# Optimization experiments

Measured on AMD Instinct MI355X. Metric: run time of the kernel, lower is better.

Reference implementation:

```python
import jax, jax.numpy as jnp
import numpy as np

B, T, M, P, N2 = 16, 8192, 128, 128, 128  # N2 = N//2 complex modes

def setup_inputs() -> dict:
    key = jax.random.key(0)
    k1, k2, k3, k4, k5 = jax.random.split(key, 5)
    u = jax.random.normal(k1, (B, T, M), dtype=jnp.float32)
    # log-parametrized Lambda (S5 'log' convention): Lambda = -exp(row0) + 1j*row1
    log_re = jnp.log(jax.random.uniform(k2, (N2,), minval=0.1, maxval=1.0))
    im = jnp.pi * jnp.arange(N2, dtype=jnp.float32)  # HiPPO-like imaginary spread
    Lambda_param = jnp.stack([log_re, im], axis=0).astype(jnp.float32)
    B_param = jax.random.normal(k3, (2, N2, M), dtype=jnp.float32) / np.sqrt(M)
    C_param = jax.random.normal(k4, (2, P, N2), dtype=jnp.float32) / np.sqrt(N2)
    delta = jnp.array([0.01], dtype=jnp.float32)  # default_\u0394
    return {"u": u, "Lambda_param": Lambda_param, "B_param": B_param,
            "C_param": C_param, "delta": delta}

def reference(u, Lambda_param, B_param, C_param, delta):
    # Reconstruct complex continuous-time matrices
    Lam = (-jnp.exp(Lambda_param[0]) + 1j * Lambda_param[1]).astype(jnp.complex64)   # (N2,)
    Bc = (B_param[0] + 1j * B_param[1]).astype(jnp.complex64)                        # (N2, M)
    Cc = (C_param[0] + 1j * C_param[1]).astype(jnp.complex64)                        # (P, N2)
    d = delta[0]
    # ZOH discretization: Lambda_d = exp(Lam*d), Bd = ((Lambda_d - 1)/Lam) * B
    Ld = jnp.exp(Lam * d)                                                            # (N2,)
    Bd = ((Ld - 1.0) / Lam)[:, None] * Bc                                            # (N2, M)
    # Input projection: Bu[b,t,n] = sum_m u[b,t,m] * Bd[n,m]
    Bu = jnp.einsum('btm,nm->btn', u.astype(jnp.complex64), Bd)                      # (B,T,N2)
    # Parallel scan of x_{k+1} = Ld * x_k + Bu_k, x_0 = 0 -> x holds x_1..x_T
    A = jnp.broadcast_to(Ld, Bu.shape)
    def comb(e1, e2):
        a1, b1 = e1
        a2, b2 = e2
        return (a1 * a2, a2 * b1 + b2)
    _, x = jax.lax.associative_scan(comb, (A, Bu), axis=1)                           # (B,T,N2)
    # return_next_y=True: y_k = 2*Re(C x_{k+1})
    y = 2.0 * jnp.real(jnp.einsum('btn,pn->btp', x, Cc))                             # (B,T,P)
    return y
```

## Files before the change

kernel.cpp:

```cpp
#include <hip/hip_runtime.h>
#include <hip/hip_bf16.h>

#define LCH 128
#define NCH 64
#define NCHUNKS 1024

typedef __attribute__((ext_vector_type(8))) short short8v;
typedef __attribute__((ext_vector_type(4))) short short4v;
typedef __attribute__((ext_vector_type(4))) float f32x4;

#define W2_LDINV 0
#define W2_LDP   16384
#define W2_E     32768
#define W2_CIN   163840
#define WS_WPACK_BYTE  2359296
#define WS_CCPACK_BYTE (2359296 + 65536)
#define WS_BUS_BYTE    (2359296 + 131072)
#define WS_NEED ((size_t)WS_BUS_BYTE + (size_t)NCHUNKS * 65536)

#define BUS_BYTE(s, np) ((((s) >> 3) * 4096) + ((np) * 16) + (((s) & 7) * 2))

__device__ inline unsigned short f2bf(float f) {
    union { __hip_bfloat16 h; unsigned short u; } v;
    v.h = __float2bfloat16(f);
    return v.u;
}
__device__ inline short4v pack4(float a, float b, float c, float d) {
    union { __hip_bfloat162 h2[2]; short4v s4; } pk;
    pk.h2[0] = __float22bfloat162_rn(make_float2(a, b));
    pk.h2[1] = __float22bfloat162_rn(make_float2(c, d));
    return pk.s4;
}

__global__ void k0_pows(const float* __restrict__ lp, const float* __restrict__ delta,
                        float2* __restrict__ ws2) {
    const int r = blockIdx.x;
    const int tid = threadIdx.x;
    const int n = tid & 127;
    const double d = (double)delta[0];
    const double lre = -exp((double)lp[n]);
    const double lim = (double)lp[128 + n];
    const double kk = (double)(r + 1) * d;
    if (tid < 128) {
        const double mag = exp(-lre * kk);
        ws2[W2_LDINV + r * 128 + n] = make_float2((float)(mag * cos(lim * kk)),
                                                  (float)(-mag * sin(lim * kk)));
    } else {
        const double mag = exp(lre * kk);
        ws2[W2_LDP + r * 128 + n] = make_float2((float)(mag * cos(lim * kk)),
                                                (float)(mag * sin(lim * kk)));
    }
}

__global__ void k0_wpack(const float* __restrict__ lp, const float* __restrict__ bp,
                         const float* __restrict__ delta, unsigned short* __restrict__ wpack) {
    const int gid = blockIdx.x * 512 + threadIdx.x;
    const int j = gid & 7;
    const int lane = (gid >> 3) & 63;
    const int ks = (gid >> 9) & 3;
    const int ntile = gid >> 11;
    const int np = ntile * 16 + (lane & 15);
    const int m = ks * 32 + ((lane >> 4) & 3) * 8 + j;
    const int n = np & 127;
    const double d = (double)delta[0];
    const double lre = -exp((double)lp[n]);
    const double lim = (double)lp[128 + n];
    const double er = exp(lre * d);
    const double ldr = er * cos(lim * d), ldi = er * sin(lim * d);
    const double nr = ldr - 1.0, ni = ldi;
    const double den = lre * lre + lim * lim;
    const double cr = (nr * lre + ni * lim) / den;
    const double ci = (ni * lre - nr * lim) / den;
    const double br = (double)bp[n * 128 + m];
    const double bi = (double)bp[16384 + n * 128 + m];
    const double v = (np < 128) ? (cr * br - ci * bi) : (cr * bi + ci * br);
    wpack[gid] = f2bf((float)v);
}

__global__ void k0_cpack(const float* __restrict__ cp, unsigned short* __restrict__ ccpack) {
    const int gid = blockIdx.x * 512 + threadIdx.x;
    const int j = gid & 7;
    const int lane = (gid >> 3) & 63;
    const int ks = (gid >> 9) & 7;
    const int ptile = gid >> 12;
    const int p = ptile * 16 + (lane & 15);
    const int k = ks * 32 + ((lane >> 4) & 3) * 8 + j;
    const int n = k >> 1;
    const float v = ((k & 1) == 0) ? 2.0f * cp[p * 128 + n] : -2.0f * cp[16384 + p * 128 + n];
    ccpack[gid] = f2bf(v);
}

__device__ inline void stage_u(const float* __restrict__ uchunk, unsigned short* lds_u) {
    const float4* uf = (const float4*)uchunk;
    const int tid = threadIdx.x;
#pragma unroll
    for (int it = 0; it < 8; ++it) {
        const int f4 = it * 512 + tid;
        const float4 v = uf[f4];
        const int t = f4 >> 5;
        const int m = (f4 & 31) * 4;
        const int byte = (t * 256 + m * 2) ^ ((t & 7) << 4);
        *(short4v*)((char*)lds_u + byte) = pack4(v.x, v.y, v.z, v.w);
    }
}

__global__ __launch_bounds__(512, 6) void k3a_bus(const float* __restrict__ u,
                                                  float2* __restrict__ ws2,
                                                  const unsigned short* __restrict__ wpack,
                                                  char* __restrict__ busg) {
    __shared__ unsigned short lds_u[16384];
    const int tid = threadIdx.x;
    const int lane = tid & 63;
    const int w = tid >> 6;
    const int tl = lane & 15;
    const int gq = (lane >> 4) & 3;
    const int g = blockIdx.x;
    const int b = g >> 6;
    const int c = g & 63;
    const int n = w * 16 + tl;
    const short8v* wp = (const short8v*)wpack;
    char* busc = busg + (size_t)g * 65536;

    stage_u(u + (size_t)(b * 8192 + c * 128) * 128, lds_u);
    __syncthreads();

    float er = 0.f, ei = 0.f;
#pragma unroll
    for (int h = 0; h < 2; ++h) {
        f32x4 acc[4][2];
#pragma unroll
        for (int i = 0; i < 4; ++i) { acc[i][0] = (f32x4)0.f; acc[i][1] = (f32x4)0.f; }
        __builtin_amdgcn_s_setprio(1);
#pragma unroll
        for (int ks = 0; ks < 4; ++ks) {
            const short8v b0 = wp[(w * 4 + ks) * 64 + lane];
            const short8v b1 = wp[((8 + w) * 4 + ks) * 64 + lane];
#pragma unroll
            for (int tt2 = 0; tt2 < 4; ++tt2) {
                const int t = (h * 4 + tt2) * 16 + tl;
                const int byte = (t * 256 + (ks * 32 + gq * 8) * 2) ^ ((t & 7) << 4);
                const short8v a = *(const short8v*)((const char*)lds_u + byte);
                acc[tt2][0] = __builtin_amdgcn_mfma_f32_16x16x32_bf16(a, b0, acc[tt2][0], 0, 0, 0);
                acc[tt2][1] = __builtin_amdgcn_mfma_f32_16x16x32_bf16(a, b1, acc[tt2][1], 0, 0, 0);
            }
        }
        __builtin_amdgcn_s_setprio(0);
        __builtin_amdgcn_sched_barrier(0);
#pragma unroll
        for (int tt2 = 0; tt2 < 4; ++tt2) {
            float vr[4], vi[4];
#pragma unroll
            for (int reg = 0; reg < 4; ++reg) {
                const int r = (h * 4 + tt2) * 16 + gq * 4 + reg;
                const float2 li = ws2[W2_LDINV + r * 128 + n];
                const float br = acc[tt2][0][reg], bi = acc[tt2][1][reg];
                vr[reg] = li.x * br - li.y * bi;
                vi[reg] = li.x * bi + li.y * br;
                er += vr[reg];
                ei += vi[reg];
            }
            const int s0 = (h * 4 + tt2) * 16 + gq * 4;
            const int rowr = w * 16 + tl;
            const int rowi = 128 + rowr;
            *(short4v*)(busc + BUS_BYTE(s0, rowr)) = pack4(vr[0], vr[1], vr[2], vr[3]);
            *(short4v*)(busc + BUS_BYTE(s0, rowi)) = pack4(vi[0], vi[1], vi[2], vi[3]);
        }
        __builtin_amdgcn_sched_barrier(0);
    }
    er += __shfl_xor(er, 16); ei += __shfl_xor(ei, 16);
    er += __shfl_xor(er, 32); ei += __shfl_xor(ei, 32);
    const float2 ld = ws2[W2_LDP + 127 * 128 + n];
    if (lane < 16) {
        ws2[W2_E + g * 128 + n] = make_float2(ld.x * er - ld.y * ei,
                                              ld.x * ei + ld.y * er);
    }
}

__global__ void k2_carry(float2* __restrict__ ws2) {
    const int idx = blockIdx.x * 256 + threadIdx.x;
    const int b = idx >> 7;
    const int n = idx & 127;
    const float2 l = ws2[W2_LDP + 127 * 128 + n];
    float cr = 0.f, ci = 0.f;
    for (int c = 0; c < NCH; ++c) {
        const int o = (b * NCH + c) * 128 + n;
        ws2[W2_CIN + o] = make_float2(cr, ci);
        const float2 e = ws2[W2_E + o];
        const float nr = fmaf(l.x, cr, fmaf(-l.y, ci, e.x));
        const float ni = fmaf(l.x, ci, fmaf(l.y, cr, e.y));
        cr = nr; ci = ni;
    }
}

__global__ __launch_bounds__(512, 4) void k3b_out(const float2* __restrict__ ws2,
                                                  const char* __restrict__ busg,
                                                  const unsigned short* __restrict__ ccpack,
                                                  float* __restrict__ y) {
    __shared__ unsigned short lds[32768];
    const int tid = threadIdx.x;
    const int lane = tid & 63;
    const int w = tid >> 6;
    const int tl = lane & 15;
    const int gq = (lane >> 4) & 3;
    const int g = blockIdx.x;
    const int b = g >> 6;
    const int c = g & 63;
    const int n = w * 16 + tl;
    const short8v* cc8 = (const short8v*)ccpack;
    const char* busc = busg + (size_t)g * 65536;

    short8v ONES, D0, D1;
#pragma unroll
    for (int j = 0; j < 8; ++j) {
        const int sl = gq * 8 + j;
        ONES[j] = (short)0x3F80;
        D0[j] = (sl <= tl) ? (short)0x3F80 : (short)0;
        D1[j] = (sl <= tl + 16) ? (short)0x3F80 : (short)0;
    }
    f32x4 z[8][2];
#pragma unroll
    for (int i = 0; i < 8; ++i) { z[i][0] = (f32x4)0.f; z[i][1] = (f32x4)0.f; }
#pragma unroll
    for (int ks = 0; ks < 4; ++ks) {
        const int sb = ks * 32 + gq * 8;
        const int rowr = w * 16 + tl;
        const int rowi = 128 + rowr;
        const short8v b0 = *(const short8v*)(busc + BUS_BYTE(sb, rowr));
        const short8v b1 = *(const short8v*)(busc + BUS_BYTE(sb, rowi));
#pragma unroll
        for (int tt = 0; tt < 8; ++tt) {
            if (tt < 2 * ks) continue;
            const short8v a = (tt == 2 * ks) ? D0 : ((tt == 2 * ks + 1) ? D1 : ONES);
            z[tt][0] = __builtin_amdgcn_mfma_f32_16x16x32_bf16(a, b0, z[tt][0], 0, 0, 0);
            z[tt][1] = __builtin_amdgcn_mfma_f32_16x16x32_bf16(a, b1, z[tt][1], 0, 0, 0);
        }
    }

    const float2 cin = ws2[W2_CIN + g * 128 + n];
#pragma unroll
    for (int tt = 0; tt < 8; ++tt) {
#pragma unroll
        for (int reg = 0; reg < 4; ++reg) {
            const int r = tt * 16 + gq * 4 + reg;
            const float2 ld = ws2[W2_LDP + r * 128 + n];
            const float zr = z[tt][0][reg] + cin.x;
            const float zi = z[tt][1][reg] + cin.y;
            const float xr = ld.x * zr - ld.y * zi;
            const float xi = ld.x * zi + ld.y * zr;
            union { __hip_bfloat162 h2; unsigned uu; } pk;
            pk.h2 = __float22bfloat162_rn(make_float2(xr, xi));
            const int byte = (r * 512 + n * 4) ^ ((r & 7) << 4);
            *(unsigned*)((char*)lds + byte) = pk.uu;
        }
    }
    __syncthreads();

    f32x4 yac[8];
#pragma unroll
    for (int i = 0; i < 8; ++i) yac[i] = (f32x4)0.f;
    __builtin_amdgcn_s_setprio(1);
#pragma unroll
    for (int ks = 0; ks < 8; ++ks) {
        const short8v bfrg = cc8[(w * 8 + ks) * 64 + lane];
#pragma unroll
        for (int tt = 0; tt < 8; ++tt) {
            const int t = tt * 16 + tl;
            const int byte = (t * 512 + (ks * 32 + gq * 8) * 2) ^ ((t & 7) << 4);
            const short8v a = *(const short8v*)((const char*)lds + byte);
            yac[tt] = __builtin_amdgcn_mfma_f32_16x16x32_bf16(a, bfrg, yac[tt], 0, 0, 0);
        }
    }
    __builtin_amdgcn_s_setprio(0);
    const int p = w * 16 + tl;
    float* yrow = y + (size_t)(b * 8192 + c * 128) * 128;
#pragma unroll
    for (int tt = 0; tt < 8; ++tt) {
#pragma unroll
        for (int reg = 0; reg < 4; ++reg) {
            const int t = tt * 16 + gq * 4 + reg;
            yrow[t * 128 + p] = yac[tt][reg];
        }
    }
}

__global__ __launch_bounds__(512, 4) void k1_end(const float* __restrict__ u,
                                                 float2* __restrict__ ws2,
                                                 const unsigned short* __restrict__ wpack) {
    __shared__ unsigned short lds_u[16384];
    const int tid = threadIdx.x;
    const int lane = tid & 63;
    const int w = tid >> 6;
    const int tl = lane & 15;
    const int gq = (lane >> 4) & 3;
    const int g = blockIdx.x;
    const int b = g >> 6;
    const int c = g & 63;
    const int n = w * 16 + tl;
    stage_u(u + (size_t)(b * 8192 + c * 128) * 128, lds_u);
    __syncthreads();
    const short8v* wp = (const short8v*)wpack;
    float er = 0.f, ei = 0.f;
#pragma unroll
    for (int h = 0; h < 2; ++h) {
        f32x4 acc[4][2];
#pragma unroll
        for (int i = 0; i < 4; ++i) { acc[i][0] = (f32x4)0.f; acc[i][1] = (f32x4)0.f; }
        __builtin_amdgcn_s_setprio(1);
#pragma unroll
        for (int ks = 0; ks < 4; ++ks) {
            const short8v b0 = wp[(w * 4 + ks) * 64 + lane];
            const short8v b1 = wp[((8 + w) * 4 + ks) * 64 + lane];
#pragma unroll
            for (int tt2 = 0; tt2 < 4; ++tt2) {
                const int t = (h * 4 + tt2) * 16 + tl;
                const int byte = (t * 256 + (ks * 32 + gq * 8) * 2) ^ ((t & 7) << 4);
                const short8v a = *(const short8v*)((const char*)lds_u + byte);
                acc[tt2][0] = __builtin_amdgcn_mfma_f32_16x16x32_bf16(a, b0, acc[tt2][0], 0, 0, 0);
                acc[tt2][1] = __builtin_amdgcn_mfma_f32_16x16x32_bf16(a, b1, acc[tt2][1], 0, 0, 0);
            }
        }
        __builtin_amdgcn_s_setprio(0);
        __builtin_amdgcn_sched_barrier(0);
#pragma unroll
        for (int tt2 = 0; tt2 < 4; ++tt2) {
#pragma unroll
            for (int reg = 0; reg < 4; ++reg) {
                const int r = (h * 4 + tt2) * 16 + gq * 4 + reg;
                const float2 li = ws2[W2_LDINV + r * 128 + n];
                const float br = acc[tt2][0][reg], bi = acc[tt2][1][reg];
                er += li.x * br - li.y * bi;
                ei += li.x * bi + li.y * br;
            }
        }
        __builtin_amdgcn_sched_barrier(0);
    }
    er += __shfl_xor(er, 16); ei += __shfl_xor(ei, 16);
    er += __shfl_xor(er, 32); ei += __shfl_xor(ei, 32);
    const float2 ld = ws2[W2_LDP + 127 * 128 + n];
    if (lane < 16) {
        ws2[W2_E + g * 128 + n] = make_float2(ld.x * er - ld.y * ei,
                                              ld.x * ei + ld.y * er);
    }
}

__global__ __launch_bounds__(512, 4) void k3_main(const float* __restrict__ u,
                                                  const float2* __restrict__ ws2,
                                                  const unsigned short* __restrict__ wpack,
                                                  const unsigned short* __restrict__ ccpack,
                                                  float* __restrict__ y) {
    __shared__ unsigned short lds[32768];
    const int tid = threadIdx.x;
    const int lane = tid & 63;
    const int w = tid >> 6;
    const int tl = lane & 15;
    const int gq = (lane >> 4) & 3;
    const int g = blockIdx.x;
    const int b = g >> 6;
    const int c = g & 63;
    const int n = w * 16 + tl;
    const short8v* wp = (const short8v*)wpack;
    const short8v* cc8 = (const short8v*)ccpack;

    stage_u(u + (size_t)(b * 8192 + c * 128) * 128, lds);
    __syncthreads();
#pragma unroll
    for (int hh = 0; hh < 2; ++hh) {
        const int h = 1 - hh;
        f32x4 acc[4][2];
#pragma unroll
        for (int i = 0; i < 4; ++i) { acc[i][0] = (f32x4)0.f; acc[i][1] = (f32x4)0.f; }
        __builtin_amdgcn_s_setprio(1);
#pragma unroll
        for (int ks = 0; ks < 4; ++ks) {
            const short8v b0 = wp[(w * 4 + ks) * 64 + lane];
            const short8v b1 = wp[((8 + w) * 4 + ks) * 64 + lane];
#pragma unroll
            for (int tt2 = 0; tt2 < 4; ++tt2) {
                const int t = (h * 4 + tt2) * 16 + tl;
                const int byte = (t * 256 + (ks * 32 + gq * 8) * 2) ^ ((t & 7) << 4);
                const short8v a = *(const short8v*)((const char*)lds + byte);
                acc[tt2][0] = __builtin_amdgcn_mfma_f32_16x16x32_bf16(a, b0, acc[tt2][0], 0, 0, 0);
                acc[tt2][1] = __builtin_amdgcn_mfma_f32_16x16x32_bf16(a, b1, acc[tt2][1], 0, 0, 0);
            }
        }
        __builtin_amdgcn_s_setprio(0);
        __builtin_amdgcn_sched_barrier(0);
        if (h == 0) __syncthreads();
#pragma unroll
        for (int tt2 = 0; tt2 < 4; ++tt2) {
            float vr[4], vi[4];
#pragma unroll
            for (int reg = 0; reg < 4; ++reg) {
                const int r = (h * 4 + tt2) * 16 + gq * 4 + reg;
                const float2 li = ws2[W2_LDINV + r * 128 + n];
                const float br = acc[tt2][0][reg], bi = acc[tt2][1][reg];
                vr[reg] = li.x * br - li.y * bi;
                vi[reg] = li.x * bi + li.y * br;
            }
            const int s0 = (h * 4 + tt2) * 16 + gq * 4;
            const int rowr = w * 16 + tl;
            const int rowi = 128 + rowr;
            *(short4v*)((char*)lds + BUS_BYTE(s0, rowr)) = pack4(vr[0], vr[1], vr[2], vr[3]);
            *(short4v*)((char*)lds + BUS_BYTE(s0, rowi)) = pack4(vi[0], vi[1], vi[2], vi[3]);
        }
        __builtin_amdgcn_sched_barrier(0);
    }
    short8v ONES, D0, D1;
#pragma unroll
    for (int j = 0; j < 8; ++j) {
        const int sl = gq * 8 + j;
        ONES[j] = (short)0x3F80;
        D0[j] = (sl <= tl) ? (short)0x3F80 : (short)0;
        D1[j] = (sl <= tl + 16) ? (short)0x3F80 : (short)0;
    }
    f32x4 z[8][2];
#pragma unroll
    for (int i = 0; i < 8; ++i) { z[i][0] = (f32x4)0.f; z[i][1] = (f32x4)0.f; }
#pragma unroll
    for (int ks = 0; ks < 4; ++ks) {
        const int sb = ks * 32 + gq * 8;
        const int rowr = w * 16 + tl;
        const int rowi = 128 + rowr;
        const short8v b0 = *(const short8v*)((const char*)lds + BUS_BYTE(sb, rowr));
        const short8v b1 = *(const short8v*)((const char*)lds + BUS_BYTE(sb, rowi));
#pragma unroll
        for (int tt = 0; tt < 8; ++tt) {
            if (tt < 2 * ks) continue;
            const short8v a = (tt == 2 * ks) ? D0 : ((tt == 2 * ks + 1) ? D1 : ONES);
            z[tt][0] = __builtin_amdgcn_mfma_f32_16x16x32_bf16(a, b0, z[tt][0], 0, 0, 0);
            z[tt][1] = __builtin_amdgcn_mfma_f32_16x16x32_bf16(a, b1, z[tt][1], 0, 0, 0);
        }
    }
    __syncthreads();
    const float2 cin = ws2[W2_CIN + g * 128 + n];
#pragma unroll
    for (int tt = 0; tt < 8; ++tt) {
#pragma unroll
        for (int reg = 0; reg < 4; ++reg) {
            const int r = tt * 16 + gq * 4 + reg;
            const float2 ld = ws2[W2_LDP + r * 128 + n];
            const float zr = z[tt][0][reg] + cin.x;
            const float zi = z[tt][1][reg] + cin.y;
            const float xr = ld.x * zr - ld.y * zi;
            const float xi = ld.x * zi + ld.y * zr;
            union { __hip_bfloat162 h2; unsigned uu; } pk;
            pk.h2 = __float22bfloat162_rn(make_float2(xr, xi));
            const int byte = (r * 512 + n * 4) ^ ((r & 7) << 4);
            *(unsigned*)((char*)lds + byte) = pk.uu;
        }
    }
    __syncthreads();
    f32x4 yac[8];
#pragma unroll
    for (int i = 0; i < 8; ++i) yac[i] = (f32x4)0.f;
    __builtin_amdgcn_s_setprio(1);
#pragma unroll
    for (int ks = 0; ks < 8; ++ks) {
        const short8v bfrg = cc8[(w * 8 + ks) * 64 + lane];
#pragma unroll
        for (int tt = 0; tt < 8; ++tt) {
            const int t = tt * 16 + tl;
            const int byte = (t * 512 + (ks * 32 + gq * 8) * 2) ^ ((t & 7) << 4);
            const short8v a = *(const short8v*)((const char*)lds + byte);
            yac[tt] = __builtin_amdgcn_mfma_f32_16x16x32_bf16(a, bfrg, yac[tt], 0, 0, 0);
        }
    }
    __builtin_amdgcn_s_setprio(0);
    const int p = w * 16 + tl;
    float* yrow = y + (size_t)(b * 8192 + c * 128) * 128;
#pragma unroll
    for (int tt = 0; tt < 8; ++tt) {
#pragma unroll
        for (int reg = 0; reg < 4; ++reg) {
            const int t = tt * 16 + gq * 4 + reg;
            yrow[t * 128 + p] = yac[tt][reg];
        }
    }
}

extern "C" void kernel_launch(void* const* d_in, const int* in_sizes, int n_in,
                              void* d_out, int out_size, void* d_ws, size_t ws_size,
                              hipStream_t stream) {
    const float* u     = (const float*)d_in[0];
    const float* lp    = (const float*)d_in[1];
    const float* bp    = (const float*)d_in[2];
    const float* cp    = (const float*)d_in[3];
    const float* delta = (const float*)d_in[4];
    float* y  = (float*)d_out;
    float2* ws2 = (float2*)d_ws;
    unsigned short* wpack  = (unsigned short*)((char*)d_ws + WS_WPACK_BYTE);
    unsigned short* ccpack = (unsigned short*)((char*)d_ws + WS_CCPACK_BYTE);
    char* busg = (char*)d_ws + WS_BUS_BYTE;

    k0_pows <<<128, 256, 0, stream>>>(lp, delta, ws2);
    k0_wpack<<<64, 512, 0, stream>>>(lp, bp, delta, wpack);
    k0_cpack<<<64, 512, 0, stream>>>(cp, ccpack);

    if (ws_size >= WS_NEED) {
        k3a_bus <<<NCHUNKS, 512, 0, stream>>>(u, ws2, wpack, busg);
        k2_carry<<<8, 256, 0, stream>>>(ws2);
        k3b_out <<<NCHUNKS, 512, 0, stream>>>(ws2, busg, ccpack, y);
    } else {
        k1_end  <<<NCHUNKS, 512, 0, stream>>>(u, ws2, wpack);
        k2_carry<<<8, 256, 0, stream>>>(ws2);
        k3_main <<<NCHUNKS, 512, 0, stream>>>(u, ws2, wpack, ccpack, y);
    }
}
```

Before: 84.32 us.

## Merge setup kernels, pipeline u staging in bus kernel, coalesce y stores via LDS

Merges the three small precompute kernels into one launch to cut launch overhead. In the Bu kernel, staging of the u chunk is split into four quarter stages with register prefetch, so global loads of the next quarter overlap the MFMA work on the current one. The output kernel now writes y through swizzled LDS and then stores coalesced float4 rows instead of scattered 4-byte stores. The cost is extra __syncthreads per quarter and an LDS round trip for the output.

```diff
diff --git a/kernel.cpp b/kernel.cpp
--- a/kernel.cpp
+++ b/kernel.cpp
@@ -32,62 +32,64 @@
     return pk.s4;
 }
 
-__global__ void k0_pows(const float* __restrict__ lp, const float* __restrict__ delta,
-                        float2* __restrict__ ws2) {
+__global__ void k0_all(const float* __restrict__ lp, const float* __restrict__ bp,
+                       const float* __restrict__ cp, const float* __restrict__ delta,
+                       float2* __restrict__ ws2, unsigned short* __restrict__ wpack,
+                       unsigned short* __restrict__ ccpack) {
     const int r = blockIdx.x;
     const int tid = threadIdx.x;
-    const int n = tid & 127;
-    const double d = (double)delta[0];
-    const double lre = -exp((double)lp[n]);
-    const double lim = (double)lp[128 + n];
-    const double kk = (double)(r + 1) * d;
-    if (tid < 128) {
-        const double mag = exp(-lre * kk);
-        ws2[W2_LDINV + r * 128 + n] = make_float2((float)(mag * cos(lim * kk)),
-                                                  (float)(-mag * sin(lim * kk)));
+    if (r < 128) {
+        if (tid < 256) {
+            const int n = tid & 127;
+            const double d = (double)delta[0];
+            const double lre = -exp((double)lp[n]);
+            const double lim = (double)lp[128 + n];
+            const double kk = (double)(r + 1) * d;
+            if (tid < 128) {
+                const double mag = exp(-lre * kk);
+                ws2[W2_LDINV + r * 128 + n] = make_float2((float)(mag * cos(lim * kk)),
+                                                          (float)(-mag * sin(lim * kk)));
+            } else {
+                const double mag = exp(lre * kk);
+                ws2[W2_LDP + r * 128 + n] = make_float2((float)(mag * cos(lim * kk)),
+                                                        (float)(mag * sin(lim * kk)));
+            }
+        }
+    } else if (r < 192) {
+        const int gid = (r - 128) * 512 + tid;
+        const int j = gid & 7;
+        const int lane = (gid >> 3) & 63;
+        const int ks = (gid >> 9) & 3;
+        const int ntile = gid >> 11;
+        const int np = ntile * 16 + (lane & 15);
+        const int m = ks * 32 + ((lane >> 4) & 3) * 8 + j;
+        const int n = np & 127;
+        const double d = (double)delta[0];
+        const double lre = -exp((double)lp[n]);
+        const double lim = (double)lp[128 + n];
+        const double er = exp(lre * d);
+        const double ldr = er * cos(lim * d), ldi = er * sin(lim * d);
+        const double nr = ldr - 1.0, ni = ldi;
+        const double den = lre * lre + lim * lim;
+        const double cr = (nr * lre + ni * lim) / den;
+        const double ci = (ni * lre - nr * lim) / den;
+        const double br = (double)bp[n * 128 + m];
+        const double bi = (double)bp[16384 + n * 128 + m];
+        const double v = (np < 128) ? (cr * br - ci * bi) : (cr * bi + ci * br);
+        wpack[gid] = f2bf((float)v);
     } else {
-        const double mag = exp(lre * kk);
-        ws2[W2_LDP + r * 128 + n] = make_float2((float)(mag * cos(lim * kk)),
-                                                (float)(mag * sin(lim * kk)));
-    }
-}
-
-__global__ void k0_wpack(const float* __restrict__ lp, const float* __restrict__ bp,
-                         const float* __restrict__ delta, unsigned short* __restrict__ wpack) {
-    const int gid = blockIdx.x * 512 + threadIdx.x;
-    const int j = gid & 7;
-    const int lane = (gid >> 3) & 63;
-    const int ks = (gid >> 9) & 3;
-    const int ntile = gid >> 11;
-    const int np = ntile * 16 + (lane & 15);
-    const int m = ks * 32 + ((lane >> 4) & 3) * 8 + j;
-    const int n = np & 127;
-    const double d = (double)delta[0];
-    const double lre = -exp((double)lp[n]);
-    const double lim = (double)lp[128 + n];
-    const double er = exp(lre * d);
-    const double ldr = er * cos(lim * d), ldi = er * sin(lim * d);
-    const double nr = ldr - 1.0, ni = ldi;
-    const double den = lre * lre + lim * lim;
-    const double cr = (nr * lre + ni * lim) / den;
-    const double ci = (ni * lre - nr * lim) / den;
-    const double br = (double)bp[n * 128 + m];
-    const double bi = (double)bp[16384 + n * 128 + m];
-    const double v = (np < 128) ? (cr * br - ci * bi) : (cr * bi + ci * br);
-    wpack[gid] = f2bf((float)v);
-}
-
-__global__ void k0_cpack(const float* __restrict__ cp, unsigned short* __restrict__ ccpack) {
-    const int gid = blockIdx.x * 512 + threadIdx.x;
-    const int j = gid & 7;
-    const int lane = (gid >> 3) & 63;
-    const int ks = (gid >> 9) & 7;
-    const int ptile = gid >> 12;
-    const int p = ptile * 16 + (lane & 15);
-    const int k = ks * 32 + ((lane >> 4) & 3) * 8 + j;
-    const int n = k >> 1;
-    const float v = ((k & 1) == 0) ? 2.0f * cp[p * 128 + n] : -2.0f * cp[16384 + p * 128 + n];
-    ccpack[gid] = f2bf(v);
+        const int gid = (r - 192) * 512 + tid;
+        const int j = gid & 7;
+        const int lane = (gid >> 3) & 63;
+        const int ks = (gid >> 9) & 7;
+        const int ptile = gid >> 12;
+        const int p = ptile * 16 + (lane & 15);
+        const int k = ks * 32 + ((lane >> 4) & 3) * 8 + j;
+        const int n = k >> 1;
+        const float v = ((k & 1) == 0) ? 2.0f * cp[p * 128 + n]
+                                       : -2.0f * cp[16384 + p * 128 + n];
+        ccpack[gid] = f2bf(v);
+    }
 }
 
 __device__ inline void stage_u(const float* __restrict__ uchunk, unsigned short* lds_u) {
@@ -118,26 +120,46 @@
     const int b = g >> 6;
     const int c = g & 63;
     const int n = w * 16 + tl;
-    const short8v* wp = (const short8v*)wpack;
     char* busc = busg + (size_t)g * 65536;
-
-    stage_u(u + (size_t)(b * 8192 + c * 128) * 128, lds_u);
-    __syncthreads();
-
+    const float4* uf = (const float4*)(u + (size_t)(b * 8192 + c * 128) * 128);
+
+    float4 pre0 = uf[tid];
+    float4 pre1 = uf[512 + tid];
     float er = 0.f, ei = 0.f;
-#pragma unroll
-    for (int h = 0; h < 2; ++h) {
-        f32x4 acc[4][2];
-#pragma unroll
-        for (int i = 0; i < 4; ++i) { acc[i][0] = (f32x4)0.f; acc[i][1] = (f32x4)0.f; }
+
+#pragma unroll
+    for (int q = 0; q < 4; ++q) {
+        {
+            const int f0 = q * 1024 + tid;
+            const int t0 = f0 >> 5, m0 = (f0 & 31) * 4;
+            *(short4v*)((char*)lds_u + ((t0 * 256 + m0 * 2) ^ ((t0 & 7) << 4))) =
+                pack4(pre0.x, pre0.y, pre0.z, pre0.w);
+            const int f1 = q * 1024 + 512 + tid;
+            const int t1 = f1 >> 5, m1 = (f1 & 31) * 4;
+            *(short4v*)((char*)lds_u + ((t1 * 256 + m1 * 2) ^ ((t1 & 7) << 4))) =
+                pack4(pre1.x, pre1.y, pre1.z, pre1.w);
+        }
+        if (q < 3) {
+            pre0 = uf[(q + 1) * 1024 + tid];
+            pre1 = uf[(q + 1) * 1024 + 512 + tid];
+        }
+        __builtin_amdgcn_sched_barrier(0);
+        __syncthreads();
+
+        unsigned long long wpu = (unsigned long long)wpack;
+        asm volatile("" : "+s"(wpu));
+        const short8v* wpq = (const short8v*)wpu;
+        f32x4 acc[2][2];
+        acc[0][0] = (f32x4)0.f; acc[0][1] = (f32x4)0.f;
+        acc[1][0] = (f32x4)0.f; acc[1][1] = (f32x4)0.f;
         __builtin_amdgcn_s_setprio(1);
 #pragma unroll
         for (int ks = 0; ks < 4; ++ks) {
-            const short8v b0 = wp[(w * 4 + ks) * 64 + lane];
-            const short8v b1 = wp[((8 + w) * 4 + ks) * 64 + lane];
-#pragma unroll
-            for (int tt2 = 0; tt2 < 4; ++tt2) {
-                const int t = (h * 4 + tt2) * 16 + tl;
+            const short8v b0 = wpq[(w * 4 + ks) * 64 + lane];
+            const short8v b1 = wpq[((8 + w) * 4 + ks) * 64 + lane];
+#pragma unroll
+            for (int tt2 = 0; tt2 < 2; ++tt2) {
+                const int t = (q * 2 + tt2) * 16 + tl;
                 const int byte = (t * 256 + (ks * 32 + gq * 8) * 2) ^ ((t & 7) << 4);
                 const short8v a = *(const short8v*)((const char*)lds_u + byte);
                 acc[tt2][0] = __builtin_amdgcn_mfma_f32_16x16x32_bf16(a, b0, acc[tt2][0], 0, 0, 0);
@@ -146,20 +168,21 @@
         }
         __builtin_amdgcn_s_setprio(0);
         __builtin_amdgcn_sched_barrier(0);
-#pragma unroll
-        for (int tt2 = 0; tt2 < 4; ++tt2) {
+
+#pragma unroll
+        for (int tt2 = 0; tt2 < 2; ++tt2) {
             float vr[4], vi[4];
 #pragma unroll
             for (int reg = 0; reg < 4; ++reg) {
-                const int r = (h * 4 + tt2) * 16 + gq * 4 + reg;
-                const float2 li = ws2[W2_LDINV + r * 128 + n];
+                const int rr = (q * 2 + tt2) * 16 + gq * 4 + reg;
+                const float2 li = ws2[W2_LDINV + rr * 128 + n];
                 const float br = acc[tt2][0][reg], bi = acc[tt2][1][reg];
                 vr[reg] = li.x * br - li.y * bi;
                 vi[reg] = li.x * bi + li.y * br;
                 er += vr[reg];
                 ei += vi[reg];
             }
-            const int s0 = (h * 4 + tt2) * 16 + gq * 4;
+            const int s0 = (q * 2 + tt2) * 16 + gq * 4;
             const int rowr = w * 16 + tl;
             const int rowi = 128 + rowr;
             *(short4v*)(busc + BUS_BYTE(s0, rowr)) = pack4(vr[0], vr[1], vr[2], vr[3]);
@@ -271,15 +294,27 @@
         }
     }
     __builtin_amdgcn_s_setprio(0);
+
+    __syncthreads();
     const int p = w * 16 + tl;
-    float* yrow = y + (size_t)(b * 8192 + c * 128) * 128;
 #pragma unroll
     for (int tt = 0; tt < 8; ++tt) {
 #pragma unroll
         for (int reg = 0; reg < 4; ++reg) {
             const int t = tt * 16 + gq * 4 + reg;
-            yrow[t * 128 + p] = yac[tt][reg];
-        }
+            const int byte = (t * 512 + p * 4) ^ ((t & 7) << 4);
+            *(float*)((char*)lds + byte) = yac[tt][reg];
+        }
+    }
+    __syncthreads();
+    float4* yf = (float4*)(y + (size_t)(b * 8192 + c * 128) * 128);
+#pragma unroll
+    for (int it = 0; it < 8; ++it) {
+        const int f4 = it * 512 + tid;
+        const int row = f4 >> 5;
+        const int col = (f4 & 31) * 4;
+        const int byte = (row * 512 + col * 4) ^ ((row & 7) << 4);
+        yf[f4] = *(float4*)((char*)lds + byte);
     }
 }
 
@@ -492,9 +527,7 @@
     unsigned short* ccpack = (unsigned short*)((char*)d_ws + WS_CCPACK_BYTE);
     char* busg = (char*)d_ws + WS_BUS_BYTE;
 
-    k0_pows <<<128, 256, 0, stream>>>(lp, delta, ws2);
-    k0_wpack<<<64, 512, 0, stream>>>(lp, bp, delta, wpack);
-    k0_cpack<<<64, 512, 0, stream>>>(cp, ccpack);
+    k0_all<<<256, 512, 0, stream>>>(lp, bp, cp, delta, ws2, wpack, ccpack);
 
     if (ws_size >= WS_NEED) {
         k3a_bus <<<NCHUNKS, 512, 0, stream>>>(u, ws2, wpack, busg);
```

Measured after the change: 87.13 us. 3.3% more time.
